# Kernel optimization log

Measured on AMD Instinct MI355X. Metric: run time of the kernel, lower is better.

The kernel has to match this reference:

```python
import jax, jax.numpy as jnp
import numpy as np

B, T, C, HS = 8, 4096, 1024, 128
BLOCK = 4096  # block_size; T == BLOCK here


def _pyr_mask(bs):
    # Faithful numpy translation of the torch 'pyr' buffer construction.
    h = bs // 2
    top = np.repeat(np.flip(np.tril(np.ones((h, h), np.float32)), axis=1), 2, axis=0)  # (bs, h)
    reps = np.array([2] * (h - 1) + [1])
    bot = np.concatenate(
        [np.zeros((1, h), np.float32),
         np.repeat(np.tril(np.ones((h, h), np.float32)), reps, axis=0)], axis=0)  # (bs, h)
    return np.concatenate([top, bot], axis=1)  # (bs, bs)


def setup_inputs() -> dict:
    key = jax.random.key(0)
    kx, kq, kk, kv = jax.random.split(key, 4)
    s = C ** -0.5
    x = jax.random.normal(kx, (B, T, C), jnp.float32)
    Wq = jax.random.normal(kq, (C, HS), jnp.float32) * s
    Wk = jax.random.normal(kk, (C, HS), jnp.float32) * s
    Wv = jax.random.normal(kv, (C, HS), jnp.float32) * s
    return {"x": x, "Wq": Wq, "Wk": Wk, "Wv": Wv}


def reference(x, Wq, Wk, Wv):
    Tlen = x.shape[1]
    start = (BLOCK - Tlen) // 2
    end = BLOCK + (-(BLOCK - Tlen)) // 2  # python floor-div, matches torch slicing
    mask = jnp.asarray(_pyr_mask(BLOCK)[:Tlen, start:end])  # (T, T) 0/1

    q = x @ Wq  # (B, T, HS)
    k = x @ Wk
    v = x @ Wv
    wei = jnp.einsum('btd,bsd->bts', q, k) * (HS ** -0.5)  # (B, T, T)
    wei = jnp.where(mask == 0, -jnp.inf, wei)  # bidirectional_mode == 'bi'
    wei = jax.nn.softmax(wei, axis=-1)
    # dropout p=0.0 -> identity
    return wei @ v  # (B, T, HS)
```

## Files before the change

kernel.cpp:

```cpp
#include <hip/hip_runtime.h>

typedef unsigned short u16;
typedef __attribute__((ext_vector_type(8))) short bf16x8;
typedef __attribute__((ext_vector_type(8))) unsigned short u16x8;
typedef __attribute__((ext_vector_type(4))) float f32x4;
typedef __attribute__((ext_vector_type(4))) unsigned short u16x4;
typedef __attribute__((ext_vector_type(2))) unsigned int u32x2;
typedef __attribute__((ext_vector_type(4))) unsigned int u32x4;

#define Bn 8
#define Tn 4096
#define Cn 1024
#define HSn 128

#define SBAR __builtin_amdgcn_sched_barrier(0)

__device__ __forceinline__ float bf2f(u16 b) {
    unsigned u = ((unsigned)b) << 16;
    return __builtin_bit_cast(float, u);
}
__device__ __forceinline__ unsigned cvt_pk_bf16(float a, float b) {
    unsigned r;
    asm("v_cvt_pk_bf16_f32 %0, %1, %2" : "=v"(r) : "v"(a), "v"(b));
    return r;
}
__device__ __forceinline__ u16 f2bf(float f) { return (u16)cvt_pk_bf16(f, f); }

__device__ __forceinline__ void wg_barrier() {
    __builtin_amdgcn_sched_barrier(0);
    asm volatile("s_waitcnt lgkmcnt(0)" ::: "memory");
    __builtin_amdgcn_s_barrier();
    __builtin_amdgcn_sched_barrier(0);
}

__device__ __forceinline__ void dma16(const void* g, void* l) {
    __builtin_amdgcn_global_load_lds(
        (const __attribute__((address_space(1))) unsigned int*)g,
        (__attribute__((address_space(3))) unsigned int*)l, 16, 0, 0);
}

extern "C" __global__ __launch_bounds__(256) void head_wtrans(
    const float* __restrict__ Wq, const float* __restrict__ Wk,
    const float* __restrict__ Wv, u16* __restrict__ wt) {
    const float* W = (blockIdx.y == 0) ? Wq : (blockIdx.y == 1) ? Wk : Wv;
    const float scale =
        (blockIdx.y == 0) ? (0.08838834764831845f * 1.4426950408889634f) : 1.0f;
    u16* o = wt + (size_t)blockIdx.y * Cn * HSn;
    int tid = blockIdx.x * 256 + threadIdx.x;
    int n = tid >> 10, kk = tid & 1023;
    o[tid] = f2bf(W[kk * HSn + n] * scale);
}

extern "C" __global__ __launch_bounds__(512) void head_proj(
    const float* __restrict__ x, const u16* __restrict__ wt, u16* __restrict__ qo,
    u16* __restrict__ ko, u16* __restrict__ vto) {
    __shared__ __align__(16) unsigned char sh[3 * 40960];
    const int tid = threadIdx.x;
    const int w = tid >> 6, l = tid & 63, quad = l >> 4, ln = l & 15;
    const int bm0 = blockIdx.x * 128;
    const int mg = w & 1, ng = w >> 1;
    const int m0 = mg * 64, n0 = ng * 96;

    const f32x4 zero4 = {0.f, 0.f, 0.f, 0.f};
    f32x4 acc[4][6];
#pragma unroll
    for (int fi = 0; fi < 4; fi++)
#pragma unroll
        for (int ci = 0; ci < 6; ci++) acc[fi][ci] = zero4;

    const float* xg[2];
    int xd[2];
#pragma unroll
    for (int p = 0; p < 2; p++) {
        int s = p * 512 + tid;
        int row = s >> 3, slot = s & 7;
        int g = slot ^ (row & 7);
        xg[p] = x + (size_t)(bm0 + row) * Cn + g * 4;
        xd[p] = s * 16;
    }
    const u16* wg[3];
    int wd[3];
#pragma unroll
    for (int p = 0; p < 3; p++) {
        int s = p * 512 + tid;
        int row = s >> 2, slot = s & 3;
        int g = slot ^ ((row >> 1) & 3);
        wg[p] = wt + (size_t)(row >> 7) * (Cn * HSn) + (size_t)(row & 127) * Cn + g * 8;
        wd[p] = 16384 + s * 16;
    }

    int aoff[4];
#pragma unroll
    for (int fi = 0; fi < 4; fi++) {
        int row = m0 + fi * 16 + ln;
        aoff[fi] = row * 128 + (((2 * quad) ^ (row & 7)) * 16);
    }
    int boff[6];
#pragma unroll
    for (int ci = 0; ci < 6; ci++) {
        int c = n0 + ci * 16 + ln;
        boff[ci] = 16384 + c * 64 + ((quad ^ ((c >> 1) & 3)) * 16);
    }

#define P_ISSUE(BUF, KT)                                      \
    do {                                                      \
        dma16(xg[0] + (KT) * 32, sh + (BUF) * 40960 + xd[0]); \
        dma16(xg[1] + (KT) * 32, sh + (BUF) * 40960 + xd[1]); \
        dma16(wg[0] + (KT) * 32, sh + (BUF) * 40960 + wd[0]); \
        dma16(wg[1] + (KT) * 32, sh + (BUF) * 40960 + wd[1]); \
        dma16(wg[2] + (KT) * 32, sh + (BUF) * 40960 + wd[2]); \
    } while (0)

#define P_COMPUTE(BUF)                                                     \
    do {                                                                   \
        const unsigned char* cbase = sh + (BUF) * 40960;                   \
        bf16x8 af[4];                                                      \
        _Pragma("unroll") for (int fi = 0; fi < 4; fi++) {                 \
            f32x4 lo = *(const f32x4*)(cbase + aoff[fi]);                  \
            f32x4 hi = *(const f32x4*)(cbase + (aoff[fi] ^ 16));           \
            u32x4 tt;                                                      \
            tt[0] = cvt_pk_bf16(lo[0], lo[1]);                             \
            tt[1] = cvt_pk_bf16(lo[2], lo[3]);                             \
            tt[2] = cvt_pk_bf16(hi[0], hi[1]);                             \
            tt[3] = cvt_pk_bf16(hi[2], hi[3]);                             \
            af[fi] = __builtin_bit_cast(bf16x8, tt);                       \
        }                                                                  \
        _Pragma("unroll") for (int ci = 0; ci < 6; ci++) {                 \
            bf16x8 bfr = *(const bf16x8*)(cbase + boff[ci]);               \
            _Pragma("unroll") for (int fi = 0; fi < 4; fi++)               \
                acc[fi][ci] = __builtin_amdgcn_mfma_f32_16x16x32_bf16(     \
                    af[fi], bfr, acc[fi][ci], 0, 0, 0);                    \
        }                                                                  \
    } while (0)

    P_ISSUE(0, 0);
    P_ISSUE(1, 1);
    P_ISSUE(2, 2);
    SBAR;
    asm volatile("s_waitcnt vmcnt(10)" ::: "memory");
    __builtin_amdgcn_s_barrier();
    SBAR;

    int cur = 0;
    for (int t = 0; t < 32; ++t) {
        P_COMPUTE(cur);
        wg_barrier();
        if (t + 3 < 32) P_ISSUE(cur, t + 3);
        SBAR;
        if (t <= 28)
            asm volatile("s_waitcnt vmcnt(10)" ::: "memory");
        else if (t == 29)
            asm volatile("s_waitcnt vmcnt(5)" ::: "memory");
        else if (t == 30)
            asm volatile("s_waitcnt vmcnt(0)" ::: "memory");
        __builtin_amdgcn_s_barrier();
        SBAR;
        cur = (cur == 2) ? 0 : cur + 1;
    }
#undef P_ISSUE
#undef P_COMPUTE

    u16* const tL = (u16*)sh;
#pragma unroll
    for (int ci = 0; ci < 6; ci++) {
        int col = n0 + ci * 16 + ln;
        int cin = col & 127;
        int sidx = col >> 7;
#pragma unroll
        for (int fi = 0; fi < 4; fi++) {
            int grow = bm0 + m0 + fi * 16 + quad * 4;
            if (sidx == 0) {
#pragma unroll
                for (int r = 0; r < 4; r++)
                    qo[(size_t)(grow + r) * HSn + cin] = f2bf(acc[fi][ci][r]);
            } else if (sidx == 1) {
#pragma unroll
                for (int r = 0; r < 4; r++)
                    ko[(size_t)(grow + r) * HSn + cin] = f2bf(acc[fi][ci][r]);
            } else {
                u16x4 pk4;
#pragma unroll
                for (int r = 0; r < 4; r++) pk4[r] = f2bf(acc[fi][ci][r]);
                *(u16x4*)(tL + cin * 136 + (m0 + fi * 16 + quad * 4)) = pk4;
            }
        }
    }
    wg_barrier();
    {
        const int bb = bm0 >> 12, t0b = bm0 & 4095;
        const int dl = tid >> 4, tch = (tid & 15) * 8;
#pragma unroll
        for (int dp = 0; dp < 4; dp++) {
            int d = dp * 32 + dl;
            u16x8 vv = *(const u16x8*)(tL + d * 136 + tch);
            *(u16x8*)(vto + ((size_t)bb * HSn + d) * Tn + t0b + tch) = vv;
        }
    }
}

extern "C" __global__ __launch_bounds__(512) void head_flash_chunk(
    const u16* __restrict__ q, const u16* __restrict__ k, const u16* __restrict__ vt,
    u16* __restrict__ Opart, float* __restrict__ lsum) {
    __shared__ __align__(16) u16 kL[64 * 136];
    __shared__ __align__(16) u16 vL[128 * 72];
    __shared__ __align__(16) u16 pL[8 * 16 * 72];
    const int tid = threadIdx.x;
    const int w = tid >> 6, l = tid & 63, quad = l >> 4, ln = l & 15;
    const int cid = blockIdx.x;
    const int grp = cid >> 4;
    const int qbi = (grp < 16) ? (31 - grp) : (grp - 16);
    const int b = (cid >> 1) & 7;
    const int half = cid & 1;
    const int q0 = qbi * 128;
    const int qrow = q0 + w * 16;

    const int rkBase = tid >> 4, ckK = tid & 15;
    const int rvBase = tid >> 3, ckV = tid & 7;

    bf16x8 qf[4];
#pragma unroll
    for (int ks = 0; ks < 4; ks++)
        qf[ks] = *(const bf16x8*)(q + ((size_t)b * Tn + qrow + ln) * HSn + ks * 32 +
                                  quad * 8);

    const f32x4 zero4 = {0.f, 0.f, 0.f, 0.f};
    float l2 = 0.f;
    const int qme = qrow + ln;
    const int clo = 2047 - (qme >> 1), chi = 2047 + ((qme + 1) >> 1);
    const int cloW0 = 2047 - (qrow >> 1);
    const int chiW0 = 2047 + ((qrow + 1) >> 1);
    const int cloMin = 2047 - ((qrow + 15) >> 1);
    const int chiMax = 2047 + ((qrow + 16) >> 1);
    f32x4 o[8];
#pragma unroll
    for (int dt = 0; dt < 8; dt++) o[dt] = zero4;

    const int qmax = q0 + 127;
    const int tlo = (2047 - (qmax >> 1)) >> 6;
    const int thi = (2047 + ((qmax + 1) >> 1)) >> 6;
    const int W = thi - tlo + 1;
    const int c0 = (W + 1) >> 1;
    const int kstart = half ? tlo + c0 : tlo;
    const int kend = half ? thi : tlo + c0 - 1;

    u16x8 pk[2], pv[2];
    {
        const int t0 = kstart * 64;
#pragma unroll
        for (int p = 0; p < 2; p++)
            pk[p] = *(const u16x8*)(k + ((size_t)b * Tn + t0 + p * 32 + rkBase) * HSn +
                                    ckK * 8);
#pragma unroll
        for (int p = 0; p < 2; p++)
            pv[p] = *(const u16x8*)(vt + ((size_t)b * HSn + p * 64 + rvBase) * Tn + t0 +
                                    ckV * 8);
    }

    for (int kt = kstart; kt <= kend; kt++) {
        const int t0 = kt * 64;
        wg_barrier();
#pragma unroll
        for (int p = 0; p < 2; p++)
            *(u16x8*)(kL + (p * 32 + rkBase) * 136 + ckK * 8) = pk[p];
#pragma unroll
        for (int p = 0; p < 2; p++)
            *(u16x8*)(vL + (p * 64 + rvBase) * 72 + ckV * 8) = pv[p];
        if (kt < kend) {
            const int t1 = t0 + 64;
#pragma unroll
            for (int p = 0; p < 2; p++)
                pk[p] = *(const u16x8*)(k + ((size_t)b * Tn + t1 + p * 32 + rkBase) * HSn +
                                        ckK * 8);
#pragma unroll
            for (int p = 0; p < 2; p++)
                pv[p] = *(const u16x8*)(vt + ((size_t)b * HSn + p * 64 + rvBase) * Tn +
                                        t1 + ckV * 8);
        }
        wg_barrier();

        const bool live = !((t0 + 63 < cloMin) || (t0 > chiMax));

        if (live) {
            f32x4 s[4];
#pragma unroll
            for (int nt = 0; nt < 4; nt++) s[nt] = zero4;
            __builtin_amdgcn_s_setprio(1);
#pragma unroll
            for (int nt = 0; nt < 4; nt++) {
                int R = nt * 16 + ln;
#pragma unroll
                for (int ks = 0; ks < 4; ks++) {
                    bf16x8 kf = *(const bf16x8*)(kL + R * 136 + (ks * 4 + quad) * 8);
                    s[nt] =
                        __builtin_amdgcn_mfma_f32_16x16x32_bf16(kf, qf[ks], s[nt], 0, 0, 0);
                }
            }
            __builtin_amdgcn_s_setprio(0);
            if (t0 < cloW0 || t0 + 63 > chiW0) {
#pragma unroll
                for (int nt = 0; nt < 4; nt++)
#pragma unroll
                    for (int r = 0; r < 4; r++) {
                        int t = t0 + nt * 16 + quad * 4 + r;
                        bool valid = (t >= clo) && (t <= chi);
                        s[nt][r] = valid ? s[nt][r] : -1e30f;
                    }
            }
            float ls = 0.f;
#pragma unroll
            for (int nt = 0; nt < 4; nt++) {
                float p0 = exp2f(s[nt][0]), p1 = exp2f(s[nt][1]);
                float p2 = exp2f(s[nt][2]), p3 = exp2f(s[nt][3]);
                ls += (p0 + p1) + (p2 + p3);
                u32x2 d;
                d.x = cvt_pk_bf16(p0, p1);
                d.y = cvt_pk_bf16(p2, p3);
                *(u32x2*)(pL + w * 1152 + ln * 72 + nt * 16 + quad * 4) = d;
            }
            l2 += ls;
            __builtin_amdgcn_s_setprio(1);
#pragma unroll
            for (int jt = 0; jt < 2; jt++) {
                bf16x8 pf = *(const bf16x8*)(pL + w * 1152 + ln * 72 + jt * 32 + quad * 8);
#pragma unroll
                for (int dt = 0; dt < 8; dt++) {
                    int R = dt * 16 + ln;
                    bf16x8 vf = *(const bf16x8*)(vL + R * 72 + (jt * 4 + quad) * 8);
                    o[dt] = __builtin_amdgcn_mfma_f32_16x16x32_bf16(pf, vf, o[dt], 0, 0, 0);
                }
            }
            __builtin_amdgcn_s_setprio(0);
        }
    }
    l2 += __shfl_xor(l2, 16, 64);
    l2 += __shfl_xor(l2, 32, 64);
#pragma unroll
    for (int dt = 0; dt < 8; dt++)
#pragma unroll
        for (int r = 0; r < 4; r++)
            Opart[((size_t)cid * 128 + w * 16 + quad * 4 + r) * HSn + dt * 16 + ln] =
                f2bf(o[dt][r]);
    if (l < 16) lsum[(size_t)cid * 128 + w * 16 + ln] = l2;
}

extern "C" __global__ __launch_bounds__(256) void head_combine(
    const u16* __restrict__ Opart, const float* __restrict__ lsum,
    float* __restrict__ out) {
    const int bid = blockIdx.x;
    const int qb64 = bid >> 3, b = bid & 7;
    const int tid = threadIdx.x;
    const int row = tid >> 2, dseg = (tid & 3) * 32;
    const int qbi = qb64 >> 1;
    const int inrow = (qb64 & 1) * 64 + row;
    const int grp0 = (qbi >= 16) ? (31 - qbi) : (qbi + 16);
    const int cid0 = grp0 * 16 + b * 2;
    const size_t r0 = (size_t)cid0 * 128 + inrow, r1 = r0 + 128;
    float l0 = lsum[r0], l1 = lsum[r1];
    float inv = 1.0f / (l0 + l1);
    float* op = out + ((size_t)b * Tn + qb64 * 64 + row) * HSn + dseg;
    const u16* p0 = Opart + r0 * HSn + dseg;
    const u16* p1 = Opart + r1 * HSn + dseg;
#pragma unroll
    for (int j = 0; j < 4; j++) {
        u16x8 a = *(const u16x8*)(p0 + j * 8);
        u16x8 c = *(const u16x8*)(p1 + j * 8);
        f32x4 o1, o2;
#pragma unroll
        for (int e = 0; e < 4; e++) o1[e] = (bf2f(a[e]) + bf2f(c[e])) * inv;
#pragma unroll
        for (int e = 0; e < 4; e++) o2[e] = (bf2f(a[4 + e]) + bf2f(c[4 + e])) * inv;
        *(f32x4*)(op + j * 8) = o1;
        *(f32x4*)(op + j * 8 + 4) = o2;
    }
}

extern "C" __global__ __launch_bounds__(256) void head_flash(
    const u16* __restrict__ q, const u16* __restrict__ k, const u16* __restrict__ vt,
    float* __restrict__ out) {
    __shared__ __align__(16) u16 kL[64 * 136];
    __shared__ __align__(16) u16 vL[128 * 72];
    __shared__ __align__(16) u16 pL[4 * 16 * 72];
    const int tid = threadIdx.x;
    const int w = tid >> 6, l = tid & 63, quad = l >> 4, ln = l & 15;
    const int bx = blockIdx.x;
    const int half = bx >> 8, idx = bx & 255;
    const int p5 = idx & 31, b = idx >> 5;
    const int qb = half ? p5 : 63 - p5;
    const int q0 = qb * 64;
    const int qrow = q0 + w * 16;
    const int rkBase = tid >> 4, ckK = tid & 15;
    const int rvBase = tid >> 3, ckV = tid & 7;

    bf16x8 qf[4];
#pragma unroll
    for (int ks = 0; ks < 4; ks++)
        qf[ks] = *(const bf16x8*)(q + ((size_t)b * Tn + qrow + ln) * HSn + ks * 32 +
                                  quad * 8);
    const f32x4 zero4 = {0.f, 0.f, 0.f, 0.f};
    float m2 = -1e30f, l2 = 0.f;
    const int qme = qrow + ln;
    const int clo = 2047 - (qme >> 1), chi = 2047 + ((qme + 1) >> 1);
    f32x4 o[8];
#pragma unroll
    for (int dt = 0; dt < 8; dt++) o[dt] = zero4;
    const int qmax = q0 + 63;
    const int tlo = (2047 - (qmax >> 1)) >> 6;
    const int thi = (2047 + ((qmax + 1) >> 1)) >> 6;

    u16x8 pk[4], pv[4];
    {
        const int t0 = tlo * 64;
#pragma unroll
        for (int p = 0; p < 4; p++)
            pk[p] = *(const u16x8*)(k + ((size_t)b * Tn + t0 + p * 16 + rkBase) * HSn +
                                    ckK * 8);
#pragma unroll
        for (int p = 0; p < 4; p++)
            pv[p] = *(const u16x8*)(vt + ((size_t)b * HSn + p * 32 + rvBase) * Tn + t0 +
                                    ckV * 8);
    }
    for (int kt = tlo; kt <= thi; kt++) {
        const int t0 = kt * 64;
        __syncthreads();
#pragma unroll
        for (int p = 0; p < 4; p++)
            *(u16x8*)(kL + (p * 16 + rkBase) * 136 + ckK * 8) = pk[p];
#pragma unroll
        for (int p = 0; p < 4; p++)
            *(u16x8*)(vL + (p * 32 + rvBase) * 72 + ckV * 8) = pv[p];
        if (kt < thi) {
            const int t1 = t0 + 64;
#pragma unroll
            for (int p = 0; p < 4; p++)
                pk[p] = *(const u16x8*)(k + ((size_t)b * Tn + t1 + p * 16 + rkBase) * HSn +
                                        ckK * 8);
#pragma unroll
            for (int p = 0; p < 4; p++)
                pv[p] = *(const u16x8*)(vt + ((size_t)b * HSn + p * 32 + rvBase) * Tn +
                                        t1 + ckV * 8);
        }
        __syncthreads();
        f32x4 s[4];
#pragma unroll
        for (int nt = 0; nt < 4; nt++) s[nt] = zero4;
#pragma unroll
        for (int nt = 0; nt < 4; nt++) {
            int R = nt * 16 + ln;
#pragma unroll
            for (int ks = 0; ks < 4; ks++) {
                bf16x8 kf = *(const bf16x8*)(kL + R * 136 + (ks * 4 + quad) * 8);
                s[nt] = __builtin_amdgcn_mfma_f32_16x16x32_bf16(kf, qf[ks], s[nt], 0, 0, 0);
            }
        }
#pragma unroll
        for (int nt = 0; nt < 4; nt++)
#pragma unroll
            for (int r = 0; r < 4; r++) {
                int t = t0 + nt * 16 + quad * 4 + r;
                bool valid = (t >= clo) && (t <= chi);
                s[nt][r] = valid ? s[nt][r] : -1e30f;
            }
        float mc = s[0][0];
#pragma unroll
        for (int nt = 0; nt < 4; nt++)
#pragma unroll
            for (int r = 0; r < 4; r++) mc = fmaxf(mc, s[nt][r]);
        mc = fmaxf(mc, __shfl_xor(mc, 16, 64));
        mc = fmaxf(mc, __shfl_xor(mc, 32, 64));
        float mn = fmaxf(m2, mc);
        float alpha = exp2f(m2 - mn);
        m2 = mn;
        float ls = 0.f;
#pragma unroll
        for (int nt = 0; nt < 4; nt++) {
            float p0 = exp2f(s[nt][0] - mn), p1 = exp2f(s[nt][1] - mn);
            float p2 = exp2f(s[nt][2] - mn), p3 = exp2f(s[nt][3] - mn);
            ls += (p0 + p1) + (p2 + p3);
            u32x2 d;
            d.x = cvt_pk_bf16(p0, p1);
            d.y = cvt_pk_bf16(p2, p3);
            *(u32x2*)(pL + w * 1152 + ln * 72 + nt * 16 + quad * 4) = d;
        }
        ls += __shfl_xor(ls, 16, 64);
        ls += __shfl_xor(ls, 32, 64);
        l2 = l2 * alpha + ls;
        float aR[4];
#pragma unroll
        for (int r = 0; r < 4; r++) aR[r] = __shfl(alpha, quad * 4 + r, 64);
#pragma unroll
        for (int dt = 0; dt < 8; dt++) {
            f32x4 oo = o[dt];
#pragma unroll
            for (int r = 0; r < 4; r++) oo[r] *= aR[r];
            o[dt] = oo;
        }
#pragma unroll
        for (int jt = 0; jt < 2; jt++) {
            bf16x8 pf = *(const bf16x8*)(pL + w * 1152 + ln * 72 + jt * 32 + quad * 8);
#pragma unroll
            for (int dt = 0; dt < 8; dt++) {
                int R = dt * 16 + ln;
                bf16x8 vf = *(const bf16x8*)(vL + R * 72 + (jt * 4 + quad) * 8);
                o[dt] = __builtin_amdgcn_mfma_f32_16x16x32_bf16(pf, vf, o[dt], 0, 0, 0);
            }
        }
    }
    float inv = 1.0f / l2;
    float rl[4];
#pragma unroll
    for (int r = 0; r < 4; r++) rl[r] = __shfl(inv, quad * 4 + r, 64);
#pragma unroll
    for (int dt = 0; dt < 8; dt++)
#pragma unroll
        for (int r = 0; r < 4; r++) {
            int row = qrow + quad * 4 + r;
            out[((size_t)b * Tn + row) * HSn + dt * 16 + ln] = o[dt][r] * rl[r];
        }
}

extern "C" void kernel_launch(void* const* d_in, const int* in_sizes, int n_in,
                              void* d_out, int out_size, void* d_ws, size_t ws_size,
                              hipStream_t stream) {
    const float* x = (const float*)d_in[0];
    const float* Wq = (const float*)d_in[1];
    const float* Wk = (const float*)d_in[2];
    const float* Wv = (const float*)d_in[3];
    float* outp = (float*)d_out;
    char* ws = (char*)d_ws;
    u16* wt = (u16*)(ws);
    u16* qb = (u16*)(ws + (1u << 20));
    u16* kb = (u16*)(ws + (9u << 20));
    u16* vtb = (u16*)(ws + (17u << 20));
    u16* Opart = (u16*)(ws + (25u << 20));
    float* lsum = (float*)(ws + (42u << 20));

    head_wtrans<<<dim3(512, 3), 256, 0, stream>>>(Wq, Wk, Wv, wt);
    head_proj<<<dim3(256), 512, 0, stream>>>(x, wt, qb, kb, vtb);
    if (ws_size >= (44ull << 20)) {
        head_flash_chunk<<<dim3(512), 512, 0, stream>>>(qb, kb, vtb, Opart, lsum);
        head_combine<<<dim3(512), 256, 0, stream>>>(Opart, lsum, outp);
    } else {
        head_flash<<<dim3(512), 256, 0, stream>>>(qb, kb, vtb, outp);
    }
}
```

Before: 297.0 us.

## Split projection into smaller blocks and widen flash chunks to 256 query rows

The projection kernel now uses 256-thread blocks covering 64 rows each, with twice as many blocks. Weight fragments load directly from global memory into registers, double-buffered, and only x goes through the LDS DMA ring. The flash-chunk kernel gives each wave 32 query rows, so every K and V fragment feeds two MFMAs. Key ranges are split into up to four 16-tile chunks per 256-row query block, skipping empty chunks, and combine sums a variable number of partials. The aim is better occupancy and K/V reuse, at the cost of more registers, a larger workspace, and a partial-sum pass that reads more data.

```diff
diff --git a/kernel.cpp b/kernel.cpp
--- a/kernel.cpp
+++ b/kernel.cpp
@@ -51,15 +51,14 @@
     o[tid] = f2bf(W[kk * HSn + n] * scale);
 }
 
-extern "C" __global__ __launch_bounds__(512) void head_proj(
+extern "C" __global__ __launch_bounds__(256) void head_proj(
     const float* __restrict__ x, const u16* __restrict__ wt, u16* __restrict__ qo,
     u16* __restrict__ ko, u16* __restrict__ vto) {
-    __shared__ __align__(16) unsigned char sh[3 * 40960];
+    __shared__ __align__(16) unsigned char sh[3 * 8192];
     const int tid = threadIdx.x;
     const int w = tid >> 6, l = tid & 63, quad = l >> 4, ln = l & 15;
-    const int bm0 = blockIdx.x * 128;
-    const int mg = w & 1, ng = w >> 1;
-    const int m0 = mg * 64, n0 = ng * 96;
+    const int bm0 = blockIdx.x * 64;
+    const int n0 = w * 96;
 
     const f32x4 zero4 = {0.f, 0.f, 0.f, 0.f};
     f32x4 acc[4][6];
@@ -72,52 +71,42 @@
     int xd[2];
 #pragma unroll
     for (int p = 0; p < 2; p++) {
-        int s = p * 512 + tid;
+        int s = p * 256 + tid;
         int row = s >> 3, slot = s & 7;
         int g = slot ^ (row & 7);
         xg[p] = x + (size_t)(bm0 + row) * Cn + g * 4;
         xd[p] = s * 16;
     }
-    const u16* wg[3];
-    int wd[3];
-#pragma unroll
-    for (int p = 0; p < 3; p++) {
-        int s = p * 512 + tid;
-        int row = s >> 2, slot = s & 3;
-        int g = slot ^ ((row >> 1) & 3);
-        wg[p] = wt + (size_t)(row >> 7) * (Cn * HSn) + (size_t)(row & 127) * Cn + g * 8;
-        wd[p] = 16384 + s * 16;
-    }
-
     int aoff[4];
 #pragma unroll
     for (int fi = 0; fi < 4; fi++) {
-        int row = m0 + fi * 16 + ln;
+        int row = fi * 16 + ln;
         aoff[fi] = row * 128 + (((2 * quad) ^ (row & 7)) * 16);
     }
-    int boff[6];
-#pragma unroll
-    for (int ci = 0; ci < 6; ci++) {
-        int c = n0 + ci * 16 + ln;
-        boff[ci] = 16384 + c * 64 + ((quad ^ ((c >> 1) & 3)) * 16);
-    }
-
-#define P_ISSUE(BUF, KT)                                      \
-    do {                                                      \
-        dma16(xg[0] + (KT) * 32, sh + (BUF) * 40960 + xd[0]); \
-        dma16(xg[1] + (KT) * 32, sh + (BUF) * 40960 + xd[1]); \
-        dma16(wg[0] + (KT) * 32, sh + (BUF) * 40960 + wd[0]); \
-        dma16(wg[1] + (KT) * 32, sh + (BUF) * 40960 + wd[1]); \
-        dma16(wg[2] + (KT) * 32, sh + (BUF) * 40960 + wd[2]); \
+    const u16* bp[6];
+#pragma unroll
+    for (int ci = 0; ci < 6; ci++)
+        bp[ci] = wt + (size_t)(n0 + ci * 16 + ln) * Cn + quad * 8;
+
+#define P_DMA(BUF, KT)                                      \
+    do {                                                    \
+        dma16(xg[0] + (KT) * 32, sh + (BUF) * 8192 + xd[0]); \
+        dma16(xg[1] + (KT) * 32, sh + (BUF) * 8192 + xd[1]); \
     } while (0)
 
-#define P_COMPUTE(BUF)                                                     \
+#define P_LOADB(DST, KT)                                                  \
+    do {                                                                  \
+        _Pragma("unroll") for (int ci = 0; ci < 6; ci++)                  \
+            DST[ci] = *(const u16x8*)(bp[ci] + (KT) * 32);                \
+    } while (0)
+
+#define P_COMPUTE(BUF, BREG)                                               \
     do {                                                                   \
-        const unsigned char* cbase = sh + (BUF) * 40960;                   \
+        const unsigned char* cb = sh + (BUF) * 8192;                       \
         bf16x8 af[4];                                                      \
         _Pragma("unroll") for (int fi = 0; fi < 4; fi++) {                 \
-            f32x4 lo = *(const f32x4*)(cbase + aoff[fi]);                  \
-            f32x4 hi = *(const f32x4*)(cbase + (aoff[fi] ^ 16));           \
+            f32x4 lo = *(const f32x4*)(cb + aoff[fi]);                     \
+            f32x4 hi = *(const f32x4*)(cb + (aoff[fi] ^ 16));              \
             u32x4 tt;                                                      \
             tt[0] = cvt_pk_bf16(lo[0], lo[1]);                             \
             tt[1] = cvt_pk_bf16(lo[2], lo[3]);                             \
@@ -126,39 +115,48 @@
             af[fi] = __builtin_bit_cast(bf16x8, tt);                       \
         }                                                                  \
         _Pragma("unroll") for (int ci = 0; ci < 6; ci++) {                 \
-            bf16x8 bfr = *(const bf16x8*)(cbase + boff[ci]);               \
+            bf16x8 bfr = __builtin_bit_cast(bf16x8, BREG[ci]);             \
             _Pragma("unroll") for (int fi = 0; fi < 4; fi++)               \
                 acc[fi][ci] = __builtin_amdgcn_mfma_f32_16x16x32_bf16(     \
                     af[fi], bfr, acc[fi][ci], 0, 0, 0);                    \
         }                                                                  \
     } while (0)
 
-    P_ISSUE(0, 0);
-    P_ISSUE(1, 1);
-    P_ISSUE(2, 2);
+#define P_BARRIER                                                  \
+    do {                                                           \
+        SBAR;                                                      \
+        asm volatile("s_waitcnt vmcnt(8) lgkmcnt(0)" ::: "memory"); \
+        __builtin_amdgcn_s_barrier();                              \
+        SBAR;                                                      \
+    } while (0)
+
+    u16x8 bA[6], bB[6];
+    P_DMA(0, 0);
+    P_DMA(1, 1);
+    P_DMA(2, 2);
+    P_LOADB(bA, 0);
     SBAR;
     asm volatile("s_waitcnt vmcnt(10)" ::: "memory");
     __builtin_amdgcn_s_barrier();
     SBAR;
 
-    int cur = 0;
-    for (int t = 0; t < 32; ++t) {
-        P_COMPUTE(cur);
-        wg_barrier();
-        if (t + 3 < 32) P_ISSUE(cur, t + 3);
-        SBAR;
-        if (t <= 28)
-            asm volatile("s_waitcnt vmcnt(10)" ::: "memory");
-        else if (t == 29)
-            asm volatile("s_waitcnt vmcnt(5)" ::: "memory");
-        else if (t == 30)
-            asm volatile("s_waitcnt vmcnt(0)" ::: "memory");
-        __builtin_amdgcn_s_barrier();
-        SBAR;
-        cur = (cur == 2) ? 0 : cur + 1;
-    }
-#undef P_ISSUE
+    int c0 = 0;
+    for (int t = 0; t < 32; t += 2) {
+        int c1 = (c0 == 2) ? 0 : c0 + 1;
+        if (t + 1 < 32) P_LOADB(bB, t + 1);
+        P_COMPUTE(c0, bA);
+        P_BARRIER;
+        if (t + 3 < 32) P_DMA(c0, t + 3);
+        if (t + 2 < 32) P_LOADB(bA, t + 2);
+        P_COMPUTE(c1, bB);
+        P_BARRIER;
+        if (t + 4 < 32) P_DMA(c1, t + 4);
+        c0 = (c1 == 2) ? 0 : c1 + 1;
+    }
+#undef P_DMA
+#undef P_LOADB
 #undef P_COMPUTE
+#undef P_BARRIER
 
     u16* const tL = (u16*)sh;
 #pragma unroll
@@ -168,7 +166,7 @@
         int sidx = col >> 7;
 #pragma unroll
         for (int fi = 0; fi < 4; fi++) {
-            int grow = bm0 + m0 + fi * 16 + quad * 4;
+            int grow = bm0 + fi * 16 + quad * 4;
             if (sidx == 0) {
 #pragma unroll
                 for (int r = 0; r < 4; r++)
@@ -181,18 +179,18 @@
                 u16x4 pk4;
 #pragma unroll
                 for (int r = 0; r < 4; r++) pk4[r] = f2bf(acc[fi][ci][r]);
-                *(u16x4*)(tL + cin * 136 + (m0 + fi * 16 + quad * 4)) = pk4;
+                *(u16x4*)(tL + cin * 80 + (fi * 16 + quad * 4)) = pk4;
             }
         }
     }
     wg_barrier();
     {
         const int bb = bm0 >> 12, t0b = bm0 & 4095;
-        const int dl = tid >> 4, tch = (tid & 15) * 8;
+        const int dl = tid >> 3, tch = (tid & 7) * 8;
 #pragma unroll
         for (int dp = 0; dp < 4; dp++) {
             int d = dp * 32 + dl;
-            u16x8 vv = *(const u16x8*)(tL + d * 136 + tch);
+            u16x8 vv = *(const u16x8*)(tL + d * 80 + tch);
             *(u16x8*)(vto + ((size_t)bb * HSn + d) * Tn + t0b + tch) = vv;
         }
     }
@@ -203,45 +201,54 @@
     u16* __restrict__ Opart, float* __restrict__ lsum) {
     __shared__ __align__(16) u16 kL[64 * 136];
     __shared__ __align__(16) u16 vL[128 * 72];
-    __shared__ __align__(16) u16 pL[8 * 16 * 72];
+    __shared__ __align__(16) u16 pL[8 * 32 * 72];
     const int tid = threadIdx.x;
     const int w = tid >> 6, l = tid & 63, quad = l >> 4, ln = l & 15;
     const int cid = blockIdx.x;
-    const int grp = cid >> 4;
-    const int qbi = (grp < 16) ? (31 - grp) : (grp - 16);
-    const int b = (cid >> 1) & 7;
-    const int half = cid & 1;
-    const int q0 = qbi * 128;
-    const int qrow = q0 + w * 16;
+    const int grp = cid >> 5;
+    const int qbi = 15 - grp;
+    const int b = (cid >> 2) & 7;
+    const int c = cid & 3;
+
+    const int q0 = qbi * 256;
+    const int qmax = q0 + 255;
+    const int tlo = (2047 - (qmax >> 1)) >> 6;
+    const int thi = (2047 + ((qmax + 1) >> 1)) >> 6;
+    const int kstart = tlo + c * 16;
+    if (kstart > thi) return;
+    const int kend = (kstart + 15 < thi) ? (kstart + 15) : thi;
+
+    const int qrow = q0 + w * 32;
 
     const int rkBase = tid >> 4, ckK = tid & 15;
     const int rvBase = tid >> 3, ckV = tid & 7;
 
-    bf16x8 qf[4];
-#pragma unroll
-    for (int ks = 0; ks < 4; ks++)
-        qf[ks] = *(const bf16x8*)(q + ((size_t)b * Tn + qrow + ln) * HSn + ks * 32 +
-                                  quad * 8);
+    bf16x8 qf[2][4];
+#pragma unroll
+    for (int g = 0; g < 2; g++)
+#pragma unroll
+        for (int ks = 0; ks < 4; ks++)
+            qf[g][ks] = *(const bf16x8*)(q + ((size_t)b * Tn + qrow + g * 16 + ln) * HSn +
+                                         ks * 32 + quad * 8);
 
     const f32x4 zero4 = {0.f, 0.f, 0.f, 0.f};
-    float l2 = 0.f;
-    const int qme = qrow + ln;
-    const int clo = 2047 - (qme >> 1), chi = 2047 + ((qme + 1) >> 1);
+    float l2[2] = {0.f, 0.f};
+    int clo[2], chi[2];
+#pragma unroll
+    for (int g = 0; g < 2; g++) {
+        int qme = qrow + g * 16 + ln;
+        clo[g] = 2047 - (qme >> 1);
+        chi[g] = 2047 + ((qme + 1) >> 1);
+    }
     const int cloW0 = 2047 - (qrow >> 1);
     const int chiW0 = 2047 + ((qrow + 1) >> 1);
-    const int cloMin = 2047 - ((qrow + 15) >> 1);
-    const int chiMax = 2047 + ((qrow + 16) >> 1);
-    f32x4 o[8];
-#pragma unroll
-    for (int dt = 0; dt < 8; dt++) o[dt] = zero4;
-
-    const int qmax = q0 + 127;
-    const int tlo = (2047 - (qmax >> 1)) >> 6;
-    const int thi = (2047 + ((qmax + 1) >> 1)) >> 6;
-    const int W = thi - tlo + 1;
-    const int c0 = (W + 1) >> 1;
-    const int kstart = half ? tlo + c0 : tlo;
-    const int kend = half ? thi : tlo + c0 - 1;
+    const int cloMin = 2047 - ((qrow + 31) >> 1);
+    const int chiMax = 2047 + ((qrow + 32) >> 1);
+    f32x4 o[2][8];
+#pragma unroll
+    for (int g = 0; g < 2; g++)
+#pragma unroll
+        for (int dt = 0; dt < 8; dt++) o[g][dt] = zero4;
 
     u16x8 pk[2], pv[2];
     {
@@ -281,9 +288,11 @@
         const bool live = !((t0 + 63 < cloMin) || (t0 > chiMax));
 
         if (live) {
-            f32x4 s[4];
-#pragma unroll
-            for (int nt = 0; nt < 4; nt++) s[nt] = zero4;
+            f32x4 s[2][4];
+#pragma unroll
+            for (int g = 0; g < 2; g++)
+#pragma unroll
+                for (int nt = 0; nt < 4; nt++) s[g][nt] = zero4;
             __builtin_amdgcn_s_setprio(1);
 #pragma unroll
             for (int nt = 0; nt < 4; nt++) {
@@ -291,56 +300,75 @@
 #pragma unroll
                 for (int ks = 0; ks < 4; ks++) {
                     bf16x8 kf = *(const bf16x8*)(kL + R * 136 + (ks * 4 + quad) * 8);
-                    s[nt] =
-                        __builtin_amdgcn_mfma_f32_16x16x32_bf16(kf, qf[ks], s[nt], 0, 0, 0);
+                    s[0][nt] =
+                        __builtin_amdgcn_mfma_f32_16x16x32_bf16(kf, qf[0][ks], s[0][nt], 0, 0, 0);
+                    s[1][nt] =
+                        __builtin_amdgcn_mfma_f32_16x16x32_bf16(kf, qf[1][ks], s[1][nt], 0, 0, 0);
                 }
             }
             __builtin_amdgcn_s_setprio(0);
             if (t0 < cloW0 || t0 + 63 > chiW0) {
 #pragma unroll
-                for (int nt = 0; nt < 4; nt++)
-#pragma unroll
-                    for (int r = 0; r < 4; r++) {
-                        int t = t0 + nt * 16 + quad * 4 + r;
-                        bool valid = (t >= clo) && (t <= chi);
-                        s[nt][r] = valid ? s[nt][r] : -1e30f;
-                    }
-            }
-            float ls = 0.f;
-#pragma unroll
-            for (int nt = 0; nt < 4; nt++) {
-                float p0 = exp2f(s[nt][0]), p1 = exp2f(s[nt][1]);
-                float p2 = exp2f(s[nt][2]), p3 = exp2f(s[nt][3]);
-                ls += (p0 + p1) + (p2 + p3);
-                u32x2 d;
-                d.x = cvt_pk_bf16(p0, p1);
-                d.y = cvt_pk_bf16(p2, p3);
-                *(u32x2*)(pL + w * 1152 + ln * 72 + nt * 16 + quad * 4) = d;
-            }
-            l2 += ls;
+                for (int g = 0; g < 2; g++)
+#pragma unroll
+                    for (int nt = 0; nt < 4; nt++)
+#pragma unroll
+                        for (int r = 0; r < 4; r++) {
+                            int t = t0 + nt * 16 + quad * 4 + r;
+                            bool valid = (t >= clo[g]) && (t <= chi[g]);
+                            s[g][nt][r] = valid ? s[g][nt][r] : -1e30f;
+                        }
+            }
+#pragma unroll
+            for (int g = 0; g < 2; g++) {
+                float ls = 0.f;
+#pragma unroll
+                for (int nt = 0; nt < 4; nt++) {
+                    float p0 = exp2f(s[g][nt][0]), p1 = exp2f(s[g][nt][1]);
+                    float p2 = exp2f(s[g][nt][2]), p3 = exp2f(s[g][nt][3]);
+                    ls += (p0 + p1) + (p2 + p3);
+                    u32x2 d;
+                    d.x = cvt_pk_bf16(p0, p1);
+                    d.y = cvt_pk_bf16(p2, p3);
+                    *(u32x2*)(pL + w * 2304 + g * 1152 + ln * 72 + nt * 16 + quad * 4) = d;
+                }
+                l2[g] += ls;
+            }
             __builtin_amdgcn_s_setprio(1);
 #pragma unroll
             for (int jt = 0; jt < 2; jt++) {
-                bf16x8 pf = *(const bf16x8*)(pL + w * 1152 + ln * 72 + jt * 32 + quad * 8);
+                bf16x8 pf0 = *(const bf16x8*)(pL + w * 2304 + ln * 72 + jt * 32 + quad * 8);
+                bf16x8 pf1 =
+                    *(const bf16x8*)(pL + w * 2304 + 1152 + ln * 72 + jt * 32 + quad * 8);
 #pragma unroll
                 for (int dt = 0; dt < 8; dt++) {
                     int R = dt * 16 + ln;
                     bf16x8 vf = *(const bf16x8*)(vL + R * 72 + (jt * 4 + quad) * 8);
-                    o[dt] = __builtin_amdgcn_mfma_f32_16x16x32_bf16(pf, vf, o[dt], 0, 0, 0);
+                    o[0][dt] = __builtin_amdgcn_mfma_f32_16x16x32_bf16(pf0, vf, o[0][dt], 0, 0, 0);
+                    o[1][dt] = __builtin_amdgcn_mfma_f32_16x16x32_bf16(pf1, vf, o[1][dt], 0, 0, 0);
                 }
             }
             __builtin_amdgcn_s_setprio(0);
         }
     }
-    l2 += __shfl_xor(l2, 16, 64);
-    l2 += __shfl_xor(l2, 32, 64);
-#pragma unroll
-    for (int dt = 0; dt < 8; dt++)
-#pragma unroll
-        for (int r = 0; r < 4; r++)
-            Opart[((size_t)cid * 128 + w * 16 + quad * 4 + r) * HSn + dt * 16 + ln] =
-                f2bf(o[dt][r]);
-    if (l < 16) lsum[(size_t)cid * 128 + w * 16 + ln] = l2;
+#pragma unroll
+    for (int g = 0; g < 2; g++) {
+        l2[g] += __shfl_xor(l2[g], 16, 64);
+        l2[g] += __shfl_xor(l2[g], 32, 64);
+    }
+#pragma unroll
+    for (int g = 0; g < 2; g++)
+#pragma unroll
+        for (int dt = 0; dt < 8; dt++)
+#pragma unroll
+            for (int r = 0; r < 4; r++)
+                Opart[((size_t)cid * 256 + w * 32 + g * 16 + quad * 4 + r) * HSn +
+                      dt * 16 + ln] = f2bf(o[g][dt][r]);
+    if (l < 16) {
+#pragma unroll
+        for (int g = 0; g < 2; g++)
+            lsum[(size_t)cid * 256 + w * 32 + g * 16 + ln] = l2[g];
+    }
 }
 
 extern "C" __global__ __launch_bounds__(256) void head_combine(
@@ -350,27 +378,37 @@
     const int qb64 = bid >> 3, b = bid & 7;
     const int tid = threadIdx.x;
     const int row = tid >> 2, dseg = (tid & 3) * 32;
-    const int qbi = qb64 >> 1;
-    const int inrow = (qb64 & 1) * 64 + row;
-    const int grp0 = (qbi >= 16) ? (31 - qbi) : (qbi + 16);
-    const int cid0 = grp0 * 16 + b * 2;
-    const size_t r0 = (size_t)cid0 * 128 + inrow, r1 = r0 + 128;
-    float l0 = lsum[r0], l1 = lsum[r1];
-    float inv = 1.0f / (l0 + l1);
-    float* op = out + ((size_t)b * Tn + qb64 * 64 + row) * HSn + dseg;
-    const u16* p0 = Opart + r0 * HSn + dseg;
-    const u16* p1 = Opart + r1 * HSn + dseg;
-#pragma unroll
-    for (int j = 0; j < 4; j++) {
-        u16x8 a = *(const u16x8*)(p0 + j * 8);
-        u16x8 c = *(const u16x8*)(p1 + j * 8);
-        f32x4 o1, o2;
-#pragma unroll
-        for (int e = 0; e < 4; e++) o1[e] = (bf2f(a[e]) + bf2f(c[e])) * inv;
-#pragma unroll
-        for (int e = 0; e < 4; e++) o2[e] = (bf2f(a[4 + e]) + bf2f(c[4 + e])) * inv;
-        *(f32x4*)(op + j * 8) = o1;
-        *(f32x4*)(op + j * 8 + 4) = o2;
+    const int gq = qb64 * 64 + row;
+    const int qbi = gq >> 8, inrow = gq & 255;
+    const int qmax = qbi * 256 + 255;
+    const int tlo = (2047 - (qmax >> 1)) >> 6;
+    const int thi = (2047 + ((qmax + 1) >> 1)) >> 6;
+    const int nc = (thi - tlo + 16) >> 4;
+    const int cid0 = (15 - qbi) * 32 + b * 4;
+
+    float accv[32];
+#pragma unroll
+    for (int e = 0; e < 32; e++) accv[e] = 0.f;
+    float lt = 0.f;
+    for (int cc = 0; cc < nc; cc++) {
+        size_t base = (size_t)(cid0 + cc) * 256 + inrow;
+        lt += lsum[base];
+        const u16* p = Opart + base * HSn + dseg;
+#pragma unroll
+        for (int j = 0; j < 4; j++) {
+            u16x8 a = *(const u16x8*)(p + j * 8);
+#pragma unroll
+            for (int e = 0; e < 8; e++) accv[j * 8 + e] += bf2f(a[e]);
+        }
+    }
+    float inv = 1.0f / lt;
+    float* op = out + ((size_t)b * Tn + gq) * HSn + dseg;
+#pragma unroll
+    for (int j = 0; j < 8; j++) {
+        f32x4 o1;
+#pragma unroll
+        for (int e = 0; e < 4; e++) o1[e] = accv[j * 4 + e] * inv;
+        *(f32x4*)(op + j * 4) = o1;
     }
 }
 
@@ -532,11 +570,11 @@
     u16* kb = (u16*)(ws + (9u << 20));
     u16* vtb = (u16*)(ws + (17u << 20));
     u16* Opart = (u16*)(ws + (25u << 20));
-    float* lsum = (float*)(ws + (42u << 20));
+    float* lsum = (float*)(ws + (58u << 20));
 
     head_wtrans<<<dim3(512, 3), 256, 0, stream>>>(Wq, Wk, Wv, wt);
-    head_proj<<<dim3(256), 512, 0, stream>>>(x, wt, qb, kb, vtb);
-    if (ws_size >= (44ull << 20)) {
+    head_proj<<<dim3(512), 256, 0, stream>>>(x, wt, qb, kb, vtb);
+    if (ws_size >= (60ull << 20)) {
         head_flash_chunk<<<dim3(512), 512, 0, stream>>>(qb, kb, vtb, Opart, lsum);
         head_combine<<<dim3(512), 256, 0, stream>>>(Opart, lsum, outp);
     } else {
```

Result: slower. 339.7 us (+14.4%).
